# Kernel tuning notes

Measured on AMD Instinct MI355X. Metric: run time of the kernel, lower is better.

Reference implementation:

```python
import jax, jax.numpy as jnp
import numpy as np

# dims
N, M, L, E = 50000, 1024, 3, 200000      # tgt nodes, src nodes, subtokens/node, edges
HID, EMB, VOCAB = 512, 256, 512
N_SLT, N_SRT = 4, 5                       # SLT edge types (messages), SRT edge types (output head)
W_SCALE = 0.02


def setup_inputs() -> dict:
    key = jax.random.key(0)
    ks = jax.random.split(key, 20)
    inp = {
        "tgt_x": jax.random.randint(ks[0], (N, L), 0, VOCAB),
        "x": jax.random.normal(ks[1], (M, HID), jnp.float32),
        "tgt_edge_index": jax.random.randint(ks[2], (2, E), 0, N),
        "tgt_edge_type": jax.random.randint(ks[3], (E,), 0, N_SLT),
        "embed_table": jax.random.normal(ks[4], (VOCAB, EMB), jnp.float32) * W_SCALE,
        # GCN layer 1 (called twice in the original forward) and layer 3 params
        "W_h1": jax.random.normal(ks[5], (EMB, EMB), jnp.float32) * W_SCALE,
        "W_rel1": jax.random.normal(ks[6], (N_SLT, EMB, EMB), jnp.float32) * W_SCALE,
        "W_src1": jax.random.normal(ks[7], (HID, EMB), jnp.float32) * W_SCALE,
        "W_h3": jax.random.normal(ks[8], (EMB, EMB), jnp.float32) * W_SCALE,
        "W_rel3": jax.random.normal(ks[9], (N_SLT, EMB, EMB), jnp.float32) * W_SCALE,
        "W_src3": jax.random.normal(ks[10], (HID, EMB), jnp.float32) * W_SCALE,
        # output heads
        "Wz": jax.random.normal(ks[11], (EMB, VOCAB), jnp.float32) * W_SCALE,
        "bz": jnp.zeros((VOCAB,), jnp.float32),
        "Wg": jax.random.normal(ks[12], (2 * EMB, N_SRT), jnp.float32) * W_SCALE,
        "bg": jnp.zeros((N_SRT,), jnp.float32),
    }
    return inp


def _gcn_layer(x_src, h, edge_index, edge_type, W_h, W_rel, W_src):
    """Relational GCN decoder layer with cross-attention to encoder nodes."""
    k = x_src @ W_src                                   # [M, EMB]
    attn = jax.nn.softmax(h @ k.T / jnp.sqrt(jnp.float32(EMB)), axis=1)  # [N, M]
    ctx = attn @ k                                      # [N, EMB]
    # per-edge-type transform first ([N, T, EMB]), then gather per edge
    h_t = jnp.einsum('nd,tdf->ntf', h, W_rel)           # [N, N_SLT, EMB]
    src, tgt = edge_index[0], edge_index[1]
    msg = h_t[src, edge_type]                           # [E, EMB] gather
    agg = jax.ops.segment_sum(msg, tgt, num_segments=h.shape[0])  # [N, EMB]
    return jax.nn.relu(h @ W_h + agg + ctx)


def reference(tgt_x, x, tgt_edge_index, tgt_edge_type, embed_table,
              W_h1, W_rel1, W_src1, W_h3, W_rel3, W_src3, Wz, bz, Wg, bg):
    # embedding + reduction over subtokens
    h = embed_table[tgt_x].sum(axis=1)                  # [N, EMB]
    # original code calls gcn1 twice, then gcn3 (gcn2 unused in training path)
    h = _gcn_layer(x, h, tgt_edge_index, tgt_edge_type, W_h1, W_rel1, W_src1)
    h = _gcn_layer(x, h, tgt_edge_index, tgt_edge_type, W_h1, W_rel1, W_src1)
    h = _gcn_layer(x, h, tgt_edge_index, tgt_edge_type, W_h3, W_rel3, W_src3)
    # node head
    node_pred = jax.nn.log_softmax(h @ Wz + bz, axis=1)  # [N, VOCAB]
    # edge head: gather [2,E,EMB] -> permute -> [E, 2*EMB]
    ef = h[tgt_edge_index]                               # [2, E, EMB]
    ef = jnp.transpose(ef, (1, 0, 2)).reshape(E, 2 * EMB)
    edge_pred = jax.nn.log_softmax(ef @ Wg + bg, axis=1)  # [E, N_SRT]
    return node_pred, edge_pred
```

## Files before the change

### kernel.cpp

```cpp
#include <hip/hip_runtime.h>
#include <hip/hip_bf16.h>
#include <cstdint>

#define N_NODES 50000
#define M_SRC   1024
#define E_EDGES 200000
#define EMB     256
#define HIDN    512
#define VOCABSZ 512

typedef __attribute__((ext_vector_type(8))) short bf16x8;
typedef __attribute__((ext_vector_type(4))) short bf16x4;
typedef __attribute__((ext_vector_type(4))) float f32x4;

__device__ inline short f2b(float f) {
    __hip_bfloat16 b = __float2bfloat16(f);
    return *reinterpret_cast<short*>(&b);
}
__device__ inline float b2f(short s) {
    __hip_bfloat16 b = *reinterpret_cast<__hip_bfloat16*>(&s);
    return __bfloat162float(b);
}

__device__ inline void tr_read2(unsigned addr, bf16x4& lo, bf16x4& hi) {
    asm volatile("ds_read_b64_tr_b16 %0, %2\n\tds_read_b64_tr_b16 %1, %2 offset:512"
                 : "=v"(lo), "=v"(hi) : "v"(addr));
}

__global__ void embed_kernel(const int* __restrict__ tgt_x,
                             const float* __restrict__ table,
                             short* __restrict__ h)
{
    int n = blockIdx.x, d = threadIdx.x;
    const int* tx = tgt_x + (size_t)n * 3;
    float s = table[(size_t)tx[0] * EMB + d]
            + table[(size_t)tx[1] * EMB + d]
            + table[(size_t)tx[2] * EMB + d];
    h[(size_t)n * EMB + d] = f2b(s);
}

__global__ void convert_kernel(const float* __restrict__ in, short* __restrict__ out, int n)
{
    int i = blockIdx.x * 256 + threadIdx.x;
    if (i * 4 < n) {
        float4 v = *(const float4*)&in[i * 4];
        short4 o;
        o.x = f2b(v.x); o.y = f2b(v.y); o.z = f2b(v.z); o.w = f2b(v.w);
        *(short4*)&out[i * 4] = o;
    }
}

template<typename TIN>
__global__ void transpose_kernel(const TIN* __restrict__ in, short* __restrict__ out, int R, int C)
{
    __shared__ float t[32][33];
    int tx = threadIdx.x & 31, ty = threadIdx.x >> 5;
    int r0 = blockIdx.y * 32, c0 = blockIdx.x * 32;
#pragma unroll
    for (int i = 0; i < 4; i++) {
        int r = ty + i * 8;
        TIN v = in[(size_t)(r0 + r) * C + c0 + tx];
        if constexpr (sizeof(TIN) == 4) t[r][tx] = v;
        else                            t[r][tx] = b2f(v);
    }
    __syncthreads();
#pragma unroll
    for (int i = 0; i < 4; i++) {
        int r = ty + i * 8;
        out[(size_t)(c0 + r) * R + r0 + tx] = f2b(t[tx][r]);
    }
}

__global__ void transposeW_kernel(const float* __restrict__ Wh1, const float* __restrict__ Wh3,
                                  const float* __restrict__ Wr1, const float* __restrict__ Wr3,
                                  short* __restrict__ WhT1, short* __restrict__ WhT3,
                                  short* __restrict__ WrT1, short* __restrict__ WrT3)
{
    __shared__ float t[32][33];
    const int z = blockIdx.z;
    const float* in; short* outp;
    if (z == 0)      { in = Wh1;                               outp = WhT1; }
    else if (z == 1) { in = Wh3;                               outp = WhT3; }
    else if (z < 6)  { in = Wr1 + (size_t)(z - 2) * EMB * EMB; outp = WrT1 + (size_t)(z - 2) * EMB * EMB; }
    else             { in = Wr3 + (size_t)(z - 6) * EMB * EMB; outp = WrT3 + (size_t)(z - 6) * EMB * EMB; }
    int tx = threadIdx.x & 31, ty = threadIdx.x >> 5;
    int r0 = blockIdx.y * 32, c0 = blockIdx.x * 32;
#pragma unroll
    for (int i = 0; i < 4; i++) {
        int r = ty + i * 8;
        t[r][tx] = in[(size_t)(r0 + r) * EMB + c0 + tx];
    }
    __syncthreads();
#pragma unroll
    for (int i = 0; i < 4; i++) {
        int r = ty + i * 8;
        outp[(size_t)(c0 + r) * EMB + r0 + tx] = f2b(t[tx][r]);
    }
}

template<int MODE>
__global__ __launch_bounds__(256) void mgemm(
    const short* __restrict__ A, const short* __restrict__ BT,
    void* __restrict__ outp, const float* __restrict__ aux,
    const float* __restrict__ bias, int NR, int K, int J)
{
    __shared__ short As[128 * 40];
    __shared__ short Bs[128 * 40];
    const int tid  = threadIdx.x;
    const int n0   = blockIdx.x * 128;
    const int j0   = blockIdx.y * 128;
    const int lane = tid & 63, wid = tid >> 6;
    const int wr   = wid >> 1, wc = wid & 1;

    f32x4 acc[4][4];
#pragma unroll
    for (int m = 0; m < 4; m++)
#pragma unroll
        for (int n = 0; n < 4; n++) acc[m][n] = (f32x4){0.f, 0.f, 0.f, 0.f};

    for (int kt = 0; kt < K; kt += 32) {
#pragma unroll
        for (int r = 0; r < 2; r++) {
            int idx = tid + r * 256;
            int row = idx >> 2, ko = (idx & 3) * 8;
            int n = n0 + row;
            bf16x8 av = {0, 0, 0, 0, 0, 0, 0, 0};
            if (n < NR) av = *(const bf16x8*)&A[(size_t)n * K + kt + ko];
            *(bf16x8*)&As[row * 40 + ko] = av;
            *(bf16x8*)&Bs[row * 40 + ko] = *(const bf16x8*)&BT[(size_t)(j0 + row) * K + kt + ko];
        }
        __syncthreads();
        bf16x8 af[4], bfr[4];
#pragma unroll
        for (int m = 0; m < 4; m++)
            af[m] = *(const bf16x8*)&As[(wr * 64 + m * 16 + (lane & 15)) * 40 + (lane >> 4) * 8];
#pragma unroll
        for (int n = 0; n < 4; n++)
            bfr[n] = *(const bf16x8*)&Bs[(wc * 64 + n * 16 + (lane & 15)) * 40 + (lane >> 4) * 8];
#pragma unroll
        for (int m = 0; m < 4; m++)
#pragma unroll
            for (int n = 0; n < 4; n++)
                acc[m][n] = __builtin_amdgcn_mfma_f32_16x16x32_bf16(af[m], bfr[n], acc[m][n], 0, 0, 0);
        __syncthreads();
    }

#pragma unroll
    for (int m = 0; m < 4; m++) {
        int rbase = wr * 64 + m * 16 + ((lane >> 4) * 4);
#pragma unroll
        for (int r = 0; r < 4; r++) {
            int n_g = n0 + rbase + r;
            if (n_g >= NR) continue;
#pragma unroll
            for (int nn = 0; nn < 4; nn++) {
                int j_g = j0 + wc * 64 + nn * 16 + (lane & 15);
                float v = acc[m][nn][r];
                if constexpr (MODE == 0) {
                    ((short*)outp)[(size_t)n_g * J + j_g] = f2b(v);
                } else {
                    float a = aux[(size_t)n_g * J + j_g];
                    ((short*)outp)[(size_t)n_g * J + j_g] = f2b(fmaxf(v + a, 0.f));
                }
            }
        }
    }
}

__global__ __launch_bounds__(256, 2) void attn_flash(
    const short* __restrict__ h, const short* __restrict__ kb,
    float* __restrict__ C, int NR)
{
    __shared__ short ks[2][32 * 256];
    __shared__ short Ps[64 * 36];

    const int tid = threadIdx.x;
    const int lane = tid & 63, wv = tid >> 6;
    const int l4 = lane >> 4, l15 = lane & 15;
    const int n0 = blockIdx.x * 64;
    const int hrow = wv * 16 + l15;

    auto LOFF = [](int key, int d8) {
        return (d8 & 1) * 8 + (key & 3) * 16 + ((key >> 3) & 3) * 64
             + ((key >> 2) & 1) * 256 + (d8 >> 1) * 512;
    };

    bf16x8 hreg[8];
    {
        int n = n0 + hrow;
        const short* hp = &h[(size_t)(n < NR ? n : 0) * 256 + l4 * 8];
#pragma unroll
        for (int kst = 0; kst < 8; kst++) hreg[kst] = *(const bf16x8*)&hp[kst * 32];
        if (n >= NR) {
#pragma unroll
            for (int kst = 0; kst < 8; kst++) hreg[kst] = (bf16x8){0, 0, 0, 0, 0, 0, 0, 0};
        }
    }

    bf16x8 rks[4];
#pragma unroll
    for (int i = 0; i < 4; i++) {
        int idx = tid + i * 256;
        rks[i] = *(const bf16x8*)&kb[(size_t)(idx >> 5) * 256 + (idx & 31) * 8];
    }
#pragma unroll
    for (int i = 0; i < 4; i++) {
        int idx = tid + i * 256;
        *(bf16x8*)&ks[0][LOFF(idx >> 5, idx & 31)] = rks[i];
    }
    __syncthreads();

    const unsigned ksbase = (unsigned)(uintptr_t)&ks[0][0];
    const unsigned trlane = 2u * (unsigned)(l15 + l4 * 64);

    f32x4 oacc[16];
#pragma unroll
    for (int mm = 0; mm < 16; mm++) oacc[mm] = (f32x4){0.f, 0.f, 0.f, 0.f};
    float lsum = 0.f;

    for (int c = 0; c < 32; c++) {
        const int cur = c & 1;
        if (c + 1 < 32) {
            const int kt0n = (c + 1) * 32;
#pragma unroll
            for (int i = 0; i < 4; i++) {
                int idx = tid + i * 256;
                rks[i] = *(const bf16x8*)&kb[(size_t)(kt0n + (idx >> 5)) * 256 + (idx & 31) * 8];
            }
        }

        f32x4 sacc[2];
        sacc[0] = (f32x4){0.f, 0.f, 0.f, 0.f};
        sacc[1] = (f32x4){0.f, 0.f, 0.f, 0.f};
#pragma unroll
        for (int kst = 0; kst < 8; kst++) {
#pragma unroll
            for (int m = 0; m < 2; m++) {
                int krow = m * 16 + l15;
                bf16x8 afk = *(const bf16x8*)&ks[cur][LOFF(krow, kst * 4 + l4)];
                sacc[m] = __builtin_amdgcn_mfma_f32_16x16x32_bf16(afk, hreg[kst], sacc[m], 0, 0, 0);
            }
        }
        float psum = 0.f;
#pragma unroll
        for (int m = 0; m < 2; m++) {
            float p0 = __expf(sacc[m][0] * 0.0625f);
            float p1 = __expf(sacc[m][1] * 0.0625f);
            float p2 = __expf(sacc[m][2] * 0.0625f);
            float p3 = __expf(sacc[m][3] * 0.0625f);
            psum += (p0 + p1) + (p2 + p3);
            short4 pk;
            pk.x = f2b(p0); pk.y = f2b(p1); pk.z = f2b(p2); pk.w = f2b(p3);
            *(short4*)&Ps[hrow * 36 + m * 16 + l4 * 4] = pk;
        }
        psum += __shfl_xor(psum, 16);
        psum += __shfl_xor(psum, 32);
        lsum += psum;

        bf16x8 bf2 = *(const bf16x8*)&Ps[(wv * 16 + l15) * 36 + l4 * 8];
        unsigned trb = ksbase + (unsigned)(cur * 16384) + trlane;
#pragma unroll
        for (int g = 0; g < 4; g++) {
            bf16x4 lo[4], hi[4];
#pragma unroll
            for (int q = 0; q < 4; q++)
                tr_read2(trb + (unsigned)((g * 4 + q) * 1024), lo[q], hi[q]);
            asm volatile("s_waitcnt lgkmcnt(0)" ::: "memory");
            __builtin_amdgcn_sched_barrier(0);
#pragma unroll
            for (int q = 0; q < 4; q++) {
                bf16x8 af2;
#pragma unroll
                for (int t2 = 0; t2 < 4; t2++) { af2[t2] = lo[q][t2]; af2[t2 + 4] = hi[q][t2]; }
                oacc[g * 4 + q] = __builtin_amdgcn_mfma_f32_16x16x32_bf16(af2, bf2, oacc[g * 4 + q], 0, 0, 0);
            }
        }

        if (c + 1 < 32) {
#pragma unroll
            for (int i = 0; i < 4; i++) {
                int idx = tid + i * 256;
                *(bf16x8*)&ks[cur ^ 1][LOFF(idx >> 5, idx & 31)] = rks[i];
            }
        }
        __syncthreads();
    }

    float li = 1.0f / lsum;
    int hr = n0 + hrow;
    if (hr < NR) {
#pragma unroll
        for (int mm = 0; mm < 16; mm++) {
            float4 v;
            v.x = oacc[mm][0] * li;
            v.y = oacc[mm][1] * li;
            v.z = oacc[mm][2] * li;
            v.w = oacc[mm][3] * li;
            *(float4*)&C[(size_t)hr * 256 + mm * 16 + l4 * 4] = v;
        }
    }
}

__global__ void hist_kernel(const int* __restrict__ ei, int* __restrict__ deg)
{
    int e = blockIdx.x * 256 + threadIdx.x;
    if (e < E_EDGES) atomicAdd(&deg[ei[E_EDGES + e]], 1);
}

__global__ void scan1_kernel(const int* __restrict__ deg, int* __restrict__ incl,
                             int* __restrict__ bsum)
{
    __shared__ int s[256];
    int i = blockIdx.x * 256 + threadIdx.x;
    int v = (i < N_NODES) ? deg[i] : 0;
    s[threadIdx.x] = v;
    __syncthreads();
#pragma unroll
    for (int off = 1; off < 256; off <<= 1) {
        int t = (threadIdx.x >= off) ? s[threadIdx.x - off] : 0;
        __syncthreads();
        s[threadIdx.x] += t;
        __syncthreads();
    }
    if (i < N_NODES) incl[i] = s[threadIdx.x];
    if (threadIdx.x == 255) bsum[blockIdx.x] = s[255];
}

__global__ void scan2_kernel(int* __restrict__ bsum, int nb)
{
    __shared__ int s[256];
    int v = (threadIdx.x < nb) ? bsum[threadIdx.x] : 0;
    s[threadIdx.x] = v;
    __syncthreads();
#pragma unroll
    for (int off = 1; off < 256; off <<= 1) {
        int t = (threadIdx.x >= off) ? s[threadIdx.x - off] : 0;
        __syncthreads();
        s[threadIdx.x] += t;
        __syncthreads();
    }
    if (threadIdx.x < nb) bsum[threadIdx.x] = s[threadIdx.x];
}

__global__ void scan3_kernel(const int* __restrict__ deg, const int* __restrict__ incl,
                             const int* __restrict__ bsum, int* __restrict__ row_ptr,
                             int* __restrict__ cursor)
{
    int i = blockIdx.x * 256 + threadIdx.x;
    if (i >= N_NODES) return;
    int pref = (blockIdx.x > 0) ? bsum[blockIdx.x - 1] : 0;
    int start = pref + incl[i] - deg[i];
    row_ptr[i] = start;
    cursor[i]  = start;
    if (i == N_NODES - 1) row_ptr[N_NODES] = pref + incl[i];
}

__global__ void fill_kernel(const int* __restrict__ ei, const int* __restrict__ et,
                            int* __restrict__ cursor, int* __restrict__ eidx)
{
    int e = blockIdx.x * 256 + threadIdx.x;
    if (e >= E_EDGES) return;
    int tg = ei[E_EDGES + e];
    int slot = atomicAdd(&cursor[tg], 1);
    eidx[slot] = ei[e] | (et[e] << 16);
}

__global__ void agg_kernel(const int* __restrict__ row_ptr, const int* __restrict__ eidx,
                           const short* __restrict__ G, float* __restrict__ C)
{
    int w = (blockIdx.x * 256 + threadIdx.x) >> 6;
    if (w >= N_NODES) return;
    int lane = threadIdx.x & 63;
    int s0 = row_ptr[w], s1 = row_ptr[w + 1];
    float a0 = 0.f, a1 = 0.f, a2 = 0.f, a3 = 0.f;
    for (int i = s0; i < s1; i++) {
        int p = eidx[i];
        int s = p & 0xFFFF, t = p >> 16;
        short4 g = *(const short4*)&G[(size_t)s * 1024 + t * 256 + lane * 4];
        a0 += b2f(g.x); a1 += b2f(g.y); a2 += b2f(g.z); a3 += b2f(g.w);
    }
    float4 c = *(float4*)&C[(size_t)w * EMB + lane * 4];
    c.x += a0; c.y += a1; c.z += a2; c.w += a3;
    *(float4*)&C[(size_t)w * EMB + lane * 4] = c;
}

__global__ __launch_bounds__(512, 2) void head_kernel(
    const short* __restrict__ hmat, const short* __restrict__ WzT,
    const float* __restrict__ bz, float* __restrict__ out, int NR)
{
    __shared__ short hs[64 * 256];
    __shared__ float redm[64 * 8];
    __shared__ float reds[64 * 8];

    const int tid = threadIdx.x;
    const int lane = tid & 63, wv = tid >> 6;
    const int l4 = lane >> 4, l15 = lane & 15;
    const int n0 = blockIdx.x * 64;

#pragma unroll
    for (int i = 0; i < 4; i++) {
        int idx = tid + i * 512;
        int row = idx >> 5, kg = idx & 31;
        bf16x8 v = {0, 0, 0, 0, 0, 0, 0, 0};
        if (n0 + row < NR) v = *(const bf16x8*)&hmat[(size_t)(n0 + row) * 256 + kg * 8];
        *(bf16x8*)&hs[(row * 256 + kg * 8) ^ ((row & 7) << 3)] = v;
    }
    __syncthreads();

    f32x4 acc[4][4];
#pragma unroll
    for (int m = 0; m < 4; m++)
#pragma unroll
        for (int n = 0; n < 4; n++) acc[m][n] = (f32x4){0.f, 0.f, 0.f, 0.f};

#pragma unroll
    for (int kt = 0; kt < 256; kt += 32) {
        bf16x8 af[4], bfr[4];
#pragma unroll
        for (int m = 0; m < 4; m++) {
            int row = m * 16 + l15;
            af[m] = *(const bf16x8*)&hs[(row * 256 + kt + l4 * 8) ^ ((row & 7) << 3)];
        }
#pragma unroll
        for (int n = 0; n < 4; n++) {
            int col = wv * 64 + n * 16 + l15;
            bfr[n] = *(const bf16x8*)&WzT[(size_t)col * 256 + kt + l4 * 8];
        }
#pragma unroll
        for (int m = 0; m < 4; m++)
#pragma unroll
            for (int n = 0; n < 4; n++)
                acc[m][n] = __builtin_amdgcn_mfma_f32_16x16x32_bf16(af[m], bfr[n], acc[m][n], 0, 0, 0);
    }

    float bcol[4];
#pragma unroll
    for (int n = 0; n < 4; n++) bcol[n] = bz[wv * 64 + n * 16 + l15];
#pragma unroll
    for (int m = 0; m < 4; m++)
#pragma unroll
        for (int n = 0; n < 4; n++)
#pragma unroll
            for (int r = 0; r < 4; r++) acc[m][n][r] += bcol[n];

    float lg[4][4];
#pragma unroll
    for (int m = 0; m < 4; m++)
#pragma unroll
        for (int r = 0; r < 4; r++) {
            float v = fmaxf(fmaxf(acc[m][0][r], acc[m][1][r]), fmaxf(acc[m][2][r], acc[m][3][r]));
            v = fmaxf(v, __shfl_xor(v, 1));
            v = fmaxf(v, __shfl_xor(v, 2));
            v = fmaxf(v, __shfl_xor(v, 4));
            v = fmaxf(v, __shfl_xor(v, 8));
            if (l15 == 0) redm[(m * 16 + l4 * 4 + r) * 8 + wv] = v;
        }
    __syncthreads();
#pragma unroll
    for (int m = 0; m < 4; m++)
#pragma unroll
        for (int r = 0; r < 4; r++) {
            int row = m * 16 + l4 * 4 + r;
            float v = redm[row * 8 + 0];
#pragma unroll
            for (int w = 1; w < 8; w++) v = fmaxf(v, redm[row * 8 + w]);
            lg[m][r] = v;
        }
#pragma unroll
    for (int m = 0; m < 4; m++)
#pragma unroll
        for (int r = 0; r < 4; r++) {
            float gm = lg[m][r];
            float s = __expf(acc[m][0][r] - gm) + __expf(acc[m][1][r] - gm)
                    + __expf(acc[m][2][r] - gm) + __expf(acc[m][3][r] - gm);
            s += __shfl_xor(s, 1);
            s += __shfl_xor(s, 2);
            s += __shfl_xor(s, 4);
            s += __shfl_xor(s, 8);
            if (l15 == 0) reds[(m * 16 + l4 * 4 + r) * 8 + wv] = s;
        }
    __syncthreads();
#pragma unroll
    for (int m = 0; m < 4; m++)
#pragma unroll
        for (int r = 0; r < 4; r++) {
            int row = m * 16 + l4 * 4 + r;
            float s = reds[row * 8 + 0];
#pragma unroll
            for (int w = 1; w < 8; w++) s += reds[row * 8 + w];
            lg[m][r] += __logf(s);
        }
#pragma unroll
    for (int m = 0; m < 4; m++)
#pragma unroll
        for (int r = 0; r < 4; r++) {
            int hr = n0 + m * 16 + l4 * 4 + r;
            if (hr >= NR) continue;
#pragma unroll
            for (int n = 0; n < 4; n++)
                out[(size_t)hr * VOCABSZ + wv * 64 + n * 16 + l15] = acc[m][n][r] - lg[m][r];
        }
}

__global__ __launch_bounds__(256) void nodeproj_kernel(
    const short* __restrict__ h, const float* __restrict__ Wg,
    float* __restrict__ eproj)
{
    int lane = threadIdx.x & 63;
    int gw   = (blockIdx.x * 256 + threadIdx.x) >> 6;
    int nw   = (gridDim.x * 256) >> 6;
    float ws[4][5], wt[4][5];
#pragma unroll
    for (int c = 0; c < 4; c++)
#pragma unroll
        for (int j = 0; j < 5; j++) {
            ws[c][j] = Wg[(size_t)(lane * 4 + c) * 5 + j];
            wt[c][j] = Wg[(size_t)(256 + lane * 4 + c) * 5 + j];
        }

    for (int n = gw; n < N_NODES; n += nw) {
        short4 hv = *(const short4*)&h[(size_t)n * EMB + lane * 4];
        float f[4] = { b2f(hv.x), b2f(hv.y), b2f(hv.z), b2f(hv.w) };
        float a[5] = {0, 0, 0, 0, 0}, b[5] = {0, 0, 0, 0, 0};
#pragma unroll
        for (int c = 0; c < 4; c++)
#pragma unroll
            for (int j = 0; j < 5; j++) {
                a[j] += f[c] * ws[c][j];
                b[j] += f[c] * wt[c][j];
            }
#pragma unroll
        for (int j = 0; j < 5; j++)
#pragma unroll
            for (int off = 32; off; off >>= 1) {
                a[j] += __shfl_xor(a[j], off);
                b[j] += __shfl_xor(b[j], off);
            }
        if (lane == 0) {
#pragma unroll
            for (int j = 0; j < 5; j++) {
                eproj[(size_t)n * 10 + j]     = a[j];
                eproj[(size_t)n * 10 + 5 + j] = b[j];
            }
        }
    }
}

__global__ void edge_lsm_kernel(const int* __restrict__ ei,
                                const float* __restrict__ eproj,
                                const float* __restrict__ bg,
                                float* __restrict__ out)
{
    int e = blockIdx.x * 256 + threadIdx.x;
    if (e >= E_EDGES) return;
    int s = ei[e], t = ei[E_EDGES + e];
    const float* ps = &eproj[(size_t)s * 10];
    const float* pt = &eproj[(size_t)t * 10 + 5];
    float z[5];
#pragma unroll
    for (int j = 0; j < 5; j++) z[j] = ps[j] + pt[j] + bg[j];
    float mm = fmaxf(fmaxf(fmaxf(z[0], z[1]), fmaxf(z[2], z[3])), z[4]);
    float ss = __expf(z[0] - mm) + __expf(z[1] - mm) + __expf(z[2] - mm)
             + __expf(z[3] - mm) + __expf(z[4] - mm);
    float lg = mm + __logf(ss);
    float* o = &out[(size_t)e * 5];
#pragma unroll
    for (int j = 0; j < 5; j++) o[j] = z[j] - lg;
}

extern "C" void kernel_launch(void* const* d_in, const int* in_sizes, int n_in,
                              void* d_out, int out_size, void* d_ws, size_t ws_size,
                              hipStream_t stream)
{
    const int*   tgt_x = (const int*)  d_in[0];
    const float* x     = (const float*)d_in[1];
    const int*   ei    = (const int*)  d_in[2];
    const int*   et    = (const int*)  d_in[3];
    const float* table = (const float*)d_in[4];
    const float* Wh1   = (const float*)d_in[5];
    const float* Wrel1 = (const float*)d_in[6];
    const float* Wsrc1 = (const float*)d_in[7];
    const float* Wh3   = (const float*)d_in[8];
    const float* Wrel3 = (const float*)d_in[9];
    const float* Wsrc3 = (const float*)d_in[10];
    const float* Wz    = (const float*)d_in[11];
    const float* bz    = (const float*)d_in[12];
    const float* Wg    = (const float*)d_in[13];
    const float* bg    = (const float*)d_in[14];
    float* out = (float*)d_out;

    short* h_a = (short*)d_ws;
    short* h_b = h_a + (size_t)N_NODES * EMB;
    float* C   = (float*)(h_b + (size_t)N_NODES * EMB);
    short* PG  = (short*)(C + (size_t)N_NODES * EMB);
    short* k1b = PG + (size_t)N_NODES * 1024;
    short* k3b = k1b + M_SRC * EMB;
    short* x_b = k3b + M_SRC * EMB;
    short* WsT1 = x_b + M_SRC * HIDN;
    short* WsT3 = WsT1 + EMB * HIDN;
    short* WhT1 = WsT3 + EMB * HIDN;
    short* WhT3 = WhT1 + EMB * EMB;
    short* WrT1 = WhT3 + EMB * EMB;
    short* WrT3 = WrT1 + 4 * EMB * EMB;
    short* WzT  = WrT3 + 4 * EMB * EMB;
    int* deg     = (int*)(WzT + VOCABSZ * EMB);
    int* incl    = deg + N_NODES;
    int* bsum    = incl + N_NODES;
    int* row_ptr = bsum + 256;
    int* cursor  = row_ptr + N_NODES + 1;
    int* eidx    = cursor + N_NODES;
    float* eproj = (float*)(eidx + E_EDGES);

    const int gN = (N_NODES + 127) / 128;
    const int gN64 = (N_NODES + 63) / 64;
    const int nb1 = (N_NODES + 255) / 256;

    hipMemsetAsync(deg, 0, N_NODES * sizeof(int), stream);
    hist_kernel<<<(E_EDGES + 255) / 256, 256, 0, stream>>>(ei, deg);
    scan1_kernel<<<nb1, 256, 0, stream>>>(deg, incl, bsum);
    scan2_kernel<<<1, 256, 0, stream>>>(bsum, nb1);
    scan3_kernel<<<nb1, 256, 0, stream>>>(deg, incl, bsum, row_ptr, cursor);
    fill_kernel<<<(E_EDGES + 255) / 256, 256, 0, stream>>>(ei, et, cursor, eidx);

    convert_kernel<<<(M_SRC * HIDN / 4 + 255) / 256, 256, 0, stream>>>(x, x_b, M_SRC * HIDN);
    transpose_kernel<float><<<dim3(EMB / 32, HIDN / 32), 256, 0, stream>>>(Wsrc1, WsT1, HIDN, EMB);
    transpose_kernel<float><<<dim3(EMB / 32, HIDN / 32), 256, 0, stream>>>(Wsrc3, WsT3, HIDN, EMB);
    transposeW_kernel<<<dim3(8, 8, 10), 256, 0, stream>>>(Wh1, Wh3, Wrel1, Wrel3,
                                                          WhT1, WhT3, WrT1, WrT3);
    transpose_kernel<float><<<dim3(VOCABSZ / 32, EMB / 32), 256, 0, stream>>>(Wz, WzT, EMB, VOCABSZ);

    mgemm<0><<<dim3(M_SRC / 128, EMB / 128), 256, 0, stream>>>(x_b, WsT1, k1b, nullptr, nullptr, M_SRC, HIDN, EMB);
    mgemm<0><<<dim3(M_SRC / 128, EMB / 128), 256, 0, stream>>>(x_b, WsT3, k3b, nullptr, nullptr, M_SRC, HIDN, EMB);

    embed_kernel<<<N_NODES, 256, 0, stream>>>(tgt_x, table, h_a);

    short* h_cur = h_a;
    short* h_nxt = h_b;
    for (int layer = 0; layer < 3; layer++) {
        const short* kb  = (layer < 2) ? k1b  : k3b;
        const short* WrT = (layer < 2) ? WrT1 : WrT3;
        const short* WhT = (layer < 2) ? WhT1 : WhT3;

        attn_flash<<<gN64, 256, 0, stream>>>(h_cur, kb, C, N_NODES);
        mgemm<0><<<dim3(gN, 8), 256, 0, stream>>>(h_cur, WrT, PG, nullptr, nullptr,
                                                  N_NODES, EMB, 4 * EMB);
        agg_kernel<<<(N_NODES + 3) / 4, 256, 0, stream>>>(row_ptr, eidx, PG, C);
        mgemm<3><<<dim3(gN, EMB / 128), 256, 0, stream>>>(h_cur, WhT, h_nxt, C, nullptr,
                                                          N_NODES, EMB, EMB);
        short* tmp = h_cur; h_cur = h_nxt; h_nxt = tmp;
    }

    head_kernel<<<gN64, 512, 0, stream>>>(h_cur, WzT, bz, out, N_NODES);

    nodeproj_kernel<<<2048, 256, 0, stream>>>(h_cur, Wg, eproj);
    edge_lsm_kernel<<<(E_EDGES + 255) / 256, 256, 0, stream>>>(ei, eproj, bg,
                                                               out + (size_t)N_NODES * VOCABSZ);
}
```

Baseline: 885.3 us.

## Stream attention keys directly to LDS with global_load_lds and batch transposed reads

```diff
diff --git a/kernel.cpp b/kernel.cpp
--- a/kernel.cpp
+++ b/kernel.cpp
@@ -22,9 +22,16 @@
     return __bfloat162float(b);
 }
 
+__device__ inline void gload16(const void* g, void* l) {
+    __builtin_amdgcn_global_load_lds(
+        (const __attribute__((address_space(1))) unsigned int*)g,
+        (__attribute__((address_space(3))) unsigned int*)l,
+        16, 0, 0);
+}
+
 __device__ inline void tr_read2(unsigned addr, bf16x4& lo, bf16x4& hi) {
     asm volatile("ds_read_b64_tr_b16 %0, %2\n\tds_read_b64_tr_b16 %1, %2 offset:512"
-                 : "=v"(lo), "=v"(hi) : "v"(addr));
+                 : "=&v"(lo), "=&v"(hi) : "v"(addr));
 }
 
 __global__ void embed_kernel(const int* __restrict__ tgt_x,
@@ -184,6 +191,13 @@
         return (d8 & 1) * 8 + (key & 3) * 16 + ((key >> 3) & 3) * 64
              + ((key >> 2) & 1) * 256 + (d8 >> 1) * 512;
     };
+    int keyq[4], d8q[4];
+#pragma unroll
+    for (int q = 0; q < 4; q++) {
+        int ci = wv * 64 + lane + q * 256;
+        d8q[q]  = (ci & 1) | ((ci >> 6) << 1);
+        keyq[q] = ((ci >> 1) & 3) | (((ci >> 5) & 1) << 2) | (((ci >> 3) & 3) << 3);
+    }
 
     bf16x8 hreg[8];
     {
@@ -197,17 +211,9 @@
         }
     }
 
-    bf16x8 rks[4];
-#pragma unroll
-    for (int i = 0; i < 4; i++) {
-        int idx = tid + i * 256;
-        rks[i] = *(const bf16x8*)&kb[(size_t)(idx >> 5) * 256 + (idx & 31) * 8];
-    }
-#pragma unroll
-    for (int i = 0; i < 4; i++) {
-        int idx = tid + i * 256;
-        *(bf16x8*)&ks[0][LOFF(idx >> 5, idx & 31)] = rks[i];
-    }
+#pragma unroll
+    for (int q = 0; q < 4; q++)
+        gload16(&kb[(size_t)keyq[q] * 256 + d8q[q] * 8], &ks[0][q * 2048 + wv * 512]);
     __syncthreads();
 
     const unsigned ksbase = (unsigned)(uintptr_t)&ks[0][0];
@@ -221,17 +227,16 @@
     for (int c = 0; c < 32; c++) {
         const int cur = c & 1;
         if (c + 1 < 32) {
-            const int kt0n = (c + 1) * 32;
-#pragma unroll
-            for (int i = 0; i < 4; i++) {
-                int idx = tid + i * 256;
-                rks[i] = *(const bf16x8*)&kb[(size_t)(kt0n + (idx >> 5)) * 256 + (idx & 31) * 8];
-            }
+            const short* kbn = kb + (size_t)(c + 1) * 32 * 256;
+#pragma unroll
+            for (int q = 0; q < 4; q++)
+                gload16(&kbn[(size_t)keyq[q] * 256 + d8q[q] * 8], &ks[cur ^ 1][q * 2048 + wv * 512]);
         }
 
         f32x4 sacc[2];
         sacc[0] = (f32x4){0.f, 0.f, 0.f, 0.f};
         sacc[1] = (f32x4){0.f, 0.f, 0.f, 0.f};
+        __builtin_amdgcn_s_setprio(1);
 #pragma unroll
         for (int kst = 0; kst < 8; kst++) {
 #pragma unroll
@@ -241,6 +246,7 @@
                 sacc[m] = __builtin_amdgcn_mfma_f32_16x16x32_bf16(afk, hreg[kst], sacc[m], 0, 0, 0);
             }
         }
+        __builtin_amdgcn_s_setprio(0);
         float psum = 0.f;
 #pragma unroll
         for (int m = 0; m < 2; m++) {
@@ -260,29 +266,24 @@
         bf16x8 bf2 = *(const bf16x8*)&Ps[(wv * 16 + l15) * 36 + l4 * 8];
         unsigned trb = ksbase + (unsigned)(cur * 16384) + trlane;
 #pragma unroll
-        for (int g = 0; g < 4; g++) {
-            bf16x4 lo[4], hi[4];
-#pragma unroll
-            for (int q = 0; q < 4; q++)
-                tr_read2(trb + (unsigned)((g * 4 + q) * 1024), lo[q], hi[q]);
+        for (int g = 0; g < 2; g++) {
+            bf16x4 lo[8], hi[8];
+#pragma unroll
+            for (int q = 0; q < 8; q++)
+                tr_read2(trb + (unsigned)((g * 8 + q) * 1024), lo[q], hi[q]);
             asm volatile("s_waitcnt lgkmcnt(0)" ::: "memory");
             __builtin_amdgcn_sched_barrier(0);
-#pragma unroll
-            for (int q = 0; q < 4; q++) {
+            __builtin_amdgcn_s_setprio(1);
+#pragma unroll
+            for (int q = 0; q < 8; q++) {
                 bf16x8 af2;
 #pragma unroll
                 for (int t2 = 0; t2 < 4; t2++) { af2[t2] = lo[q][t2]; af2[t2 + 4] = hi[q][t2]; }
-                oacc[g * 4 + q] = __builtin_amdgcn_mfma_f32_16x16x32_bf16(af2, bf2, oacc[g * 4 + q], 0, 0, 0);
+                oacc[g * 8 + q] = __builtin_amdgcn_mfma_f32_16x16x32_bf16(af2, bf2, oacc[g * 8 + q], 0, 0, 0);
             }
-        }
-
-        if (c + 1 < 32) {
-#pragma unroll
-            for (int i = 0; i < 4; i++) {
-                int idx = tid + i * 256;
-                *(bf16x8*)&ks[cur ^ 1][LOFF(idx >> 5, idx & 31)] = rks[i];
-            }
-        }
+            __builtin_amdgcn_s_setprio(0);
+        }
+
         __syncthreads();
     }
 
```

New measurement: 895.0 us. About the same (+1.1%).
